# Kernel optimization log

Hardware: AMD Instinct MI355X
Metric: run time of the kernel (lower is better)

Reference implementation:

```python
import jax, jax.numpy as jnp
import numpy as np

B, T, D = 2, 2048, 1024
NH, NKV, HD, RD = 16, 4, 64, 32


def apply_rope(x, cos, sin):
    # x: [B, H, T, hd]; cos/sin: [T, 1, 1, RD//2]
    r = cos.shape[-1] * 2
    x1 = x[..., : r // 2]
    x2 = x[..., r // 2 : r]
    x_pass = x[..., r:]
    c = cos.reshape(1, 1, cos.shape[0], -1)  # [1,1,T,RD//2]
    s = sin.reshape(1, 1, sin.shape[0], -1)
    return jnp.concatenate([x1 * c - x2 * s, x1 * s + x2 * c, x_pass], axis=-1)


def setup_inputs() -> dict:
    key = jax.random.key(0)
    ks = jax.random.split(key, 8)
    # realistic partial-RoPE angle tables
    inv_freq = 1.0 / (10000.0 ** (np.arange(0, RD, 2, dtype=np.float32) / RD))
    ang = np.arange(T, dtype=np.float32)[:, None] * inv_freq[None, :]  # [T, RD//2]
    cos = jnp.asarray(np.cos(ang)).reshape(T, 1, 1, RD // 2)
    sin = jnp.asarray(np.sin(ang)).reshape(T, 1, 1, RD // 2)
    return {
        "x": jax.random.normal(ks[0], (B, T, D), dtype=jnp.float32),
        "cos": cos,
        "sin": sin,
        "v0": jax.random.normal(ks[1], (B, NH, T, HD), dtype=jnp.float32),
        "Wqkv": jax.random.normal(ks[2], ((NH + 2 * NKV) * HD, D), dtype=jnp.float32) * (D ** -0.5),
        "Wproj": jax.random.normal(ks[3], (D, D), dtype=jnp.float32) * (D ** -0.5),
        "vrl_alpha": jnp.full((NH,), 0.1, dtype=jnp.float32),
        "qk_scale": 0.5 + jax.random.uniform(ks[4], (NH,), dtype=jnp.float32),
    }


def reference(x, cos, sin, v0, Wqkv, Wproj, vrl_alpha, qk_scale):
    nH, nKV, hd = NH, NKV, HD
    qkv = jnp.einsum("btd,ed->bte", x, Wqkv)  # [B,T,(nH+2nKV)*hd]
    q = qkv[..., : nH * hd].reshape(B, T, nH, hd).transpose(0, 2, 1, 3)
    k = qkv[..., nH * hd : (nH + nKV) * hd].reshape(B, T, nKV, hd).transpose(0, 2, 1, 3)
    v = qkv[..., (nH + nKV) * hd :].reshape(B, T, nKV, hd).transpose(0, 2, 1, 3)
    q = apply_rope(q, cos, sin)
    k = apply_rope(k, cos, sin)
    reps = nH // nKV
    k_exp = jnp.repeat(k, reps, axis=1)  # [B,nH,T,hd]
    v_exp = jnp.repeat(v, reps, axis=1)
    # VRL blend (layer_idx > 0)
    alpha = jax.nn.sigmoid(vrl_alpha)[None, :, None, None]
    v_exp = (1.0 - alpha) * v_exp + alpha * v0
    # per-head learned qk scale, split as sqrt on q and k
    sfac = jnp.sqrt(qk_scale[None, :, None, None] * (hd ** -0.5))
    q_s = q * sfac
    k_s = k_exp * sfac
    # causal SDPA (default scale 1/sqrt(hd))
    scores = jnp.einsum("bhqd,bhkd->bhqk", q_s, k_s) * (hd ** -0.5)
    causal = jnp.tril(jnp.ones((T, T), dtype=bool))
    scores = jnp.where(causal[None, None], scores, jnp.float32(-1e30))
    attn = jax.nn.softmax(scores, axis=-1)
    y = jnp.einsum("bhqk,bhkd->bhqd", attn, v_exp)
    y = y.transpose(0, 2, 1, 3).reshape(B, T, D)
    out = jnp.einsum("btd,ed->bte", y, Wproj)
    return out, v0
```

## Files before the change

kernel.cpp:

```cpp
#include <hip/hip_runtime.h>
#include <hip/hip_bf16.h>

#define B_   2
#define T_   2048
#define D_   1024
#define NH_  16
#define NKV_ 4
#define HD_  64
#define E_   1536
#define LOG2E 1.4426950408889634f

typedef __attribute__((ext_vector_type(8))) __bf16 bf16x8;
typedef __attribute__((ext_vector_type(4))) __bf16 bf16x4;
typedef __attribute__((ext_vector_type(4))) float f32x4;

static __device__ __forceinline__ void gld_lds16(const unsigned short* g, unsigned short* l) {
  __builtin_amdgcn_global_load_lds(
      (const __attribute__((address_space(1))) unsigned int*)(unsigned long long)(const void*)g,
      (__attribute__((address_space(3))) unsigned int*)(unsigned int)(unsigned long long)(void*)l,
      16, 0, 0);
}

static __device__ __forceinline__ float fexp2(float x) {
  float r; asm("v_exp_f32 %0, %1" : "=v"(r) : "v"(x)); return r;
}
static __device__ __forceinline__ float fmax3(float a, float b, float c) {
  float r; asm("v_max3_f32 %0, %1, %2, %3" : "=v"(r) : "v"(a), "v"(b), "v"(c)); return r;
}
static __device__ __forceinline__ float frcp(float x) {
  float r; asm("v_rcp_f32 %0, %1" : "=v"(r) : "v"(x)); return r;
}

#define CVT8(dst, f0, f1) {                                                    \
  dst[0] = (__bf16)f0.x; dst[1] = (__bf16)f0.y;                               \
  dst[2] = (__bf16)f0.z; dst[3] = (__bf16)f0.w;                               \
  dst[4] = (__bf16)f1.x; dst[5] = (__bf16)f1.y;                               \
  dst[6] = (__bf16)f1.z; dst[7] = (__bf16)f1.w; }

__global__ void k_convert_all(const float* __restrict__ x, const float* __restrict__ wq,
                              const float* __restrict__ wp,
                              unsigned short* __restrict__ xb, unsigned short* __restrict__ wqb,
                              unsigned short* __restrict__ wpb) {
  int i = blockIdx.x * blockDim.x + threadIdx.x;
  const float* src; unsigned short* dst; int j;
  if (i < 524288)      { src = x;  dst = xb;  j = i; }
  else if (i < 720896) { src = wq; dst = wqb; j = i - 524288; }
  else                 { src = wp; dst = wpb; j = i - 720896; }
  int n = j >> 7, c8 = (j & 127) * 8;
  const float4* p = (const float4*)(src + (size_t)n * 1024 + c8);
  float4 a = p[0], b = p[1];
  bf16x8 o; CVT8(o, a, b);
  *(bf16x8*)(dst + (size_t)n * 1024 + (c8 ^ ((n & 7) * 8))) = o;
}

__global__ __launch_bounds__(256) void k_gemm_qkv(
    const unsigned short* __restrict__ A,
    const unsigned short* __restrict__ W,
    const float* __restrict__ cosT, const float* __restrict__ sinT,
    const float* __restrict__ v0,
    const float* __restrict__ vrl, const float* __restrict__ qks,
    unsigned short* __restrict__ qb, unsigned short* __restrict__ kb,
    unsigned short* __restrict__ vb) {
  __shared__ __align__(16) unsigned short As[2][128 * 64];
  __shared__ __align__(16) unsigned short Ws[2][64 * 64];
  int tid = threadIdx.x;
  int w = tid >> 6, l = tid & 63, lo = l & 15, hi = l >> 4;
  int f = blockIdx.y * 24 + blockIdx.x;
  int f2 = (f & 7) * 96 + (f >> 3);
  int bn = f2 % 24, bm = f2 / 24;
  int rsw = (lo & 7) * 8;

  const unsigned short* Ab = A + (size_t)bm * 128 * 1024;
  const unsigned short* Wb = W + (size_t)bn * 64 * 1024;

  f32x4 acc[2][4];
#pragma unroll
  for (int mi = 0; mi < 2; ++mi)
#pragma unroll
    for (int ni = 0; ni < 4; ++ni) acc[mi][ni] = (f32x4){0.f, 0.f, 0.f, 0.f};

#define STAGE(kt, buf) {                                                       \
  int k0 = (kt) * 64;                                                         \
  _Pragma("unroll") for (int ii = 0; ii < 4; ++ii) {                          \
    int sb = ii * 256 + w * 64;                                               \
    gld_lds16(Ab + (size_t)((sb + l) >> 3) * 1024 + k0 + ((sb + l) & 7) * 8,  \
              &As[buf][sb * 8]); }                                            \
  _Pragma("unroll") for (int ii = 0; ii < 2; ++ii) {                          \
    int sb = ii * 256 + w * 64;                                               \
    gld_lds16(Wb + (size_t)((sb + l) >> 3) * 1024 + k0 + ((sb + l) & 7) * 8,  \
              &Ws[buf][sb * 8]); } }

  STAGE(0, 0);
  __syncthreads();

  for (int kt = 0; kt < 16; ++kt) {
    int cur = kt & 1;
    bool pf = (kt + 1) < 16;
    if (pf) STAGE(kt + 1, cur ^ 1);
    __builtin_amdgcn_s_setprio(1);
#pragma unroll
    for (int kk = 0; kk < 2; ++kk) {
      int c0 = (kk * 32 + hi * 8) ^ rsw;
      bf16x8 af0 = *(const bf16x8*)&As[cur][(w * 32 + lo) * 64 + c0];
      bf16x8 af1 = *(const bf16x8*)&As[cur][(w * 32 + 16 + lo) * 64 + c0];
#pragma unroll
      for (int ni = 0; ni < 4; ++ni) {
        bf16x8 wf = *(const bf16x8*)&Ws[cur][(ni * 16 + lo) * 64 + c0];
        acc[0][ni] = __builtin_amdgcn_mfma_f32_16x16x32_bf16(af0, wf, acc[0][ni], 0, 0, 0);
        acc[1][ni] = __builtin_amdgcn_mfma_f32_16x16x32_bf16(af1, wf, acc[1][ni], 0, 0, 0);
      }
    }
    __builtin_amdgcn_s_setprio(0);
    __syncthreads();
  }
#undef STAGE

  if (bn < 20) {
    int isq = (bn < 16);
    int h = isq ? bn : bn - 16;
    float sc = isq ? (qks[h] * (LOG2E / 64.0f)) : 1.0f;
    unsigned short* base = isq ? qb : kb;
    int nheads = isq ? NH_ : NKV_;
#pragma unroll
    for (int mi = 0; mi < 2; ++mi) {
#pragma unroll
      for (int r = 0; r < 4; ++r) {
        int row = bm * 128 + w * 32 + mi * 16 + hi * 4 + r;
        int b = row >> 11, t = row & 2047;
        float c = cosT[t * 16 + lo], s = sinT[t * 16 + lo];
        float a0 = acc[mi][0][r], a1 = acc[mi][1][r];
        __bf16* dp = (__bf16*)(base + ((size_t)(b * nheads + h) * T_ + t) * 64);
        int ts = isq ? 0 : (8 * (t & 7));
        dp[lo ^ ts]        = (__bf16)((a0 * c - a1 * s) * sc);
        dp[(16 + lo) ^ ts] = (__bf16)((a0 * s + a1 * c) * sc);
        dp[(32 + lo) ^ ts] = (__bf16)(acc[mi][2][r] * sc);
        dp[(48 + lo) ^ ts] = (__bf16)(acc[mi][3][r] * sc);
      }
    }
  } else {
    int hv = bn - 20;
    float av[4];
#pragma unroll
    for (int j = 0; j < 4; ++j) av[j] = 1.0f / (1.0f + __expf(-vrl[hv * 4 + j]));
#pragma unroll
    for (int mi = 0; mi < 2; ++mi) {
      int t0g = bm * 128 + w * 32 + mi * 16 + hi * 4;
      int b = t0g >> 11, t0 = t0g & 2047;
#pragma unroll
      for (int ni = 0; ni < 4; ++ni) {
        int d = ni * 16 + lo;
#pragma unroll
        for (int j = 0; j < 4; ++j) {
          float a = av[j], na = 1.0f - a;
          const float* v0p = v0 + ((size_t)(b * NH_ + hv * 4 + j) * T_ + t0) * 64 + d;
          bf16x4 vv;
#pragma unroll
          for (int r = 0; r < 4; ++r)
            vv[r] = (__bf16)(na * acc[mi][ni][r] + a * v0p[(size_t)r * 64]);
          *(bf16x4*)((unsigned short*)vb + ((size_t)(b * NH_ + hv * 4 + j) * 64 + d) * T_ +
                     (t0 ^ (8 * (lo & 7)))) = vv;
        }
      }
    }
  }
}

__global__ __launch_bounds__(256) void k_gemm_proj(
    const unsigned short* __restrict__ A,
    const unsigned short* __restrict__ W,
    const float* __restrict__ v0,
    float* __restrict__ C, float* __restrict__ out2) {
  __shared__ __align__(16) unsigned short As[2][128 * 64];
  __shared__ __align__(16) unsigned short Ws[2][64 * 64];
  int tid = threadIdx.x;

  if (blockIdx.y >= 32) {
    int idx = ((blockIdx.y - 32) * 16 + blockIdx.x) * 256 + tid;
    const float4* src = (const float4*)v0;
    float4* dst = (float4*)out2;
#pragma unroll
    for (int i = 0; i < 32; ++i) dst[idx + i * 32768] = src[idx + i * 32768];
    return;
  }

  int w = tid >> 6, l = tid & 63, lo = l & 15, hi = l >> 4;
  int f = blockIdx.y * 16 + blockIdx.x;
  int f2 = (f & 7) * 64 + (f >> 3);
  int bn = f2 & 15, bm = f2 >> 4;
  int rsw = (lo & 7) * 8;

  const unsigned short* Ab = A + (size_t)bm * 128 * 1024;
  const unsigned short* Wb = W + (size_t)bn * 64 * 1024;

  f32x4 acc[2][4];
#pragma unroll
  for (int mi = 0; mi < 2; ++mi)
#pragma unroll
    for (int ni = 0; ni < 4; ++ni) acc[mi][ni] = (f32x4){0.f, 0.f, 0.f, 0.f};

#define STAGE(kt, buf) {                                                       \
  int k0 = (kt) * 64;                                                         \
  _Pragma("unroll") for (int ii = 0; ii < 4; ++ii) {                          \
    int sb = ii * 256 + w * 64;                                               \
    gld_lds16(Ab + (size_t)((sb + l) >> 3) * 1024 + k0 + ((sb + l) & 7) * 8,  \
              &As[buf][sb * 8]); }                                            \
  _Pragma("unroll") for (int ii = 0; ii < 2; ++ii) {                          \
    int sb = ii * 256 + w * 64;                                               \
    gld_lds16(Wb + (size_t)((sb + l) >> 3) * 1024 + k0 + ((sb + l) & 7) * 8,  \
              &Ws[buf][sb * 8]); } }

  STAGE(0, 0);
  __syncthreads();
  for (int kt = 0; kt < 16; ++kt) {
    int cur = kt & 1;
    bool pf = (kt + 1) < 16;
    if (pf) STAGE(kt + 1, cur ^ 1);
    __builtin_amdgcn_s_setprio(1);
#pragma unroll
    for (int kk = 0; kk < 2; ++kk) {
      int c0 = (kk * 32 + hi * 8) ^ rsw;
      bf16x8 af0 = *(const bf16x8*)&As[cur][(w * 32 + lo) * 64 + c0];
      bf16x8 af1 = *(const bf16x8*)&As[cur][(w * 32 + 16 + lo) * 64 + c0];
#pragma unroll
      for (int ni = 0; ni < 4; ++ni) {
        bf16x8 wf = *(const bf16x8*)&Ws[cur][(ni * 16 + lo) * 64 + c0];
        acc[0][ni] = __builtin_amdgcn_mfma_f32_16x16x32_bf16(af0, wf, acc[0][ni], 0, 0, 0);
        acc[1][ni] = __builtin_amdgcn_mfma_f32_16x16x32_bf16(af1, wf, acc[1][ni], 0, 0, 0);
      }
    }
    __builtin_amdgcn_s_setprio(0);
    __syncthreads();
  }
#undef STAGE

#pragma unroll
  for (int mi = 0; mi < 2; ++mi) {
#pragma unroll
    for (int r = 0; r < 4; ++r) {
      int row = bm * 128 + w * 32 + mi * 16 + hi * 4 + r;
      float* cp = C + (size_t)row * D_ + bn * 64 + lo;
#pragma unroll
      for (int ni = 0; ni < 4; ++ni) cp[ni * 16] = acc[mi][ni][r];
    }
  }
}

static __device__ __forceinline__ void stage_kv8(const unsigned short* Kb, const unsigned short* Vb,
                                                 int kv0, int w, int l,
                                                 unsigned short* KsB, unsigned short* VsB) {
  gld_lds16(Kb + (size_t)kv0 * 64 + w * 512 + l * 8, KsB + w * 512);
  gld_lds16(Vb + (size_t)(w * 8 + (l >> 3)) * T_ + kv0 + (l & 7) * 8, VsB + w * 512);
}

__device__ __forceinline__ void softmax_state(f32x4 (&s)[4], float& m, float& lsum,
                                              f32x4 (&y)[4], unsigned short* PsW,
                                              int lo, int hi, int swz) {
  float a0 = fmax3(s[0][0], s[0][1], s[0][2]);
  float a1 = fmax3(s[0][3], s[1][0], s[1][1]);
  float a2 = fmax3(s[1][2], s[1][3], s[2][0]);
  float a3 = fmax3(s[2][1], s[2][2], s[2][3]);
  float a4 = fmax3(s[3][0], s[3][1], s[3][2]);
  float pm = fmaxf(fmax3(a0, a1, a2), fmax3(a3, a4, s[3][3]));
  if (!__all(pm <= m + 8.0f)) {
    pm = fmaxf(pm, __shfl_xor(pm, 16));
    pm = fmaxf(pm, __shfl_xor(pm, 32));
    float mnew = fmaxf(m, pm);
    float sc = fexp2(m - mnew);
    lsum *= sc;
#pragma unroll
    for (int r = 0; r < 4; ++r) {
      float scr = __shfl(sc, hi * 4 + r);
#pragma unroll
      for (int nf = 0; nf < 4; ++nf) y[nf][r] *= scr;
    }
    m = mnew;
  }
  float rs = 0.f;
#pragma unroll
  for (int nt = 0; nt < 4; ++nt) {
    float p0 = fexp2(s[nt][0] - m);
    float p1 = fexp2(s[nt][1] - m);
    float p2 = fexp2(s[nt][2] - m);
    float p3 = fexp2(s[nt][3] - m);
    rs += (p0 + p1) + (p2 + p3);
    bf16x4 pk;
    pk[0] = (__bf16)p0; pk[1] = (__bf16)p1; pk[2] = (__bf16)p2; pk[3] = (__bf16)p3;
    *(bf16x4*)(PsW + lo * 64 + ((nt * 16 + hi * 4) ^ swz)) = pk;
  }
  lsum += rs;
}

__global__ __launch_bounds__(512, 4) void k_attn(const unsigned short* __restrict__ Q,
                                                 const unsigned short* __restrict__ Kp,
                                                 const unsigned short* __restrict__ Vtp,
                                                 unsigned short* __restrict__ Y) {
  int p = blockIdx.x, h = blockIdx.y, b = blockIdx.z;
  if (b == 1) p = 15 - p;
  int tid = threadIdx.x;
  int w = tid >> 6, l = tid & 63, lo = l & 15, hi = l >> 4;
  int kh = h >> 2;
  int qtA = p, qtB = 31 - p;
  int ntB = qtB + 1;
  int st = w >> 2, wq = w & 3;
  int qt = st ? qtA : qtB;
  int q0 = qt * 64 + wq * 16;
  int swz = 8 * (lo & 7);

  __shared__ __align__(16) unsigned short Ks[2][4096];
  __shared__ __align__(16) unsigned short Vs[2][4096];
  __shared__ __align__(16) unsigned short Ps[8192];
  unsigned short* PsW = &Ps[w * 1024];

  const unsigned short* Qb = Q + ((size_t)(b * NH_ + h) * T_) * 64;
  const unsigned short* Kb = Kp + ((size_t)(b * NKV_ + kh) * T_) * 64;
  const unsigned short* Vb = Vtp + ((size_t)(b * NH_ + h) * 64) * T_;

  bf16x8 q_0 = *(const bf16x8*)(Qb + (size_t)(q0 + lo) * 64 + hi * 8);
  bf16x8 q_1 = *(const bf16x8*)(Qb + (size_t)(q0 + lo) * 64 + 32 + hi * 8);

  f32x4 y[4];
#pragma unroll
  for (int nf = 0; nf < 4; ++nf) y[nf] = (f32x4){0.f, 0.f, 0.f, 0.f};
  float m = -INFINITY, lsum = 0.f;

  stage_kv8(Kb, Vb, 0, w, l, Ks[0], Vs[0]);
  __syncthreads();
  int cur = 0;

  for (int kt = 0; kt < ntB; ++kt) {
    bool pf = (kt + 1) < ntB;
    if (pf) stage_kv8(Kb, Vb, (kt + 1) * 64, w, l, Ks[cur ^ 1], Vs[cur ^ 1]);

    if (kt <= qt) {
      int kv0 = kt * 64;
      const unsigned short* KsC = Ks[cur];
      const unsigned short* VsC = Vs[cur];

      f32x4 s[4];
      __builtin_amdgcn_s_setprio(1);
#pragma unroll
      for (int nt = 0; nt < 4; ++nt) {
        int rrow = (nt * 16 + lo) * 64;
        int c0 = (hi * 8) ^ swz;
        bf16x8 kf0 = *(const bf16x8*)&KsC[rrow + c0];
        bf16x8 kf1 = *(const bf16x8*)&KsC[rrow + (c0 ^ 32)];
        f32x4 a = (f32x4){0.f, 0.f, 0.f, 0.f};
        a = __builtin_amdgcn_mfma_f32_16x16x32_bf16(kf0, q_0, a, 0, 0, 0);
        a = __builtin_amdgcn_mfma_f32_16x16x32_bf16(kf1, q_1, a, 0, 0, 0);
        s[nt] = a;
      }
      __builtin_amdgcn_s_setprio(0);

      if (kt == qt) {
#pragma unroll
        for (int nt = 0; nt < 4; ++nt)
#pragma unroll
          for (int r = 0; r < 4; ++r)
            if (kv0 + nt * 16 + hi * 4 + r > q0 + lo) s[nt][r] = -1e30f;
      }

      softmax_state(s, m, lsum, y, PsW, lo, hi, swz);

      __builtin_amdgcn_s_setprio(1);
#pragma unroll
      for (int kc = 0; kc < 2; ++kc) {
        int pcol = (kc * 32 + hi * 8) ^ swz;
        bf16x8 pa = *(const bf16x8*)&PsW[lo * 64 + pcol];
#pragma unroll
        for (int nf = 0; nf < 4; ++nf) {
          bf16x8 vf = *(const bf16x8*)&VsC[(nf * 16 + lo) * 64 + pcol];
          y[nf] = __builtin_amdgcn_mfma_f32_16x16x32_bf16(pa, vf, y[nf], 0, 0, 0);
        }
      }
      __builtin_amdgcn_s_setprio(0);
    }

    __syncthreads();
    cur ^= 1;
  }

  lsum += __shfl_xor(lsum, 16);
  lsum += __shfl_xor(lsum, 32);
  float inv = frcp(lsum);
#pragma unroll
  for (int r = 0; r < 4; ++r) {
    float iv = __shfl(inv, hi * 4 + r);
    int t = q0 + hi * 4 + r;
    int sw = 8 * (t & 7);
    __bf16* yp = (__bf16*)(Y + ((size_t)(b * T_ + t)) * D_ + h * 64);
#pragma unroll
    for (int nf = 0; nf < 4; ++nf)
      yp[(nf * 16 + lo) ^ sw] = (__bf16)(y[nf][r] * iv);
  }
}

extern "C" void kernel_launch(void* const* d_in, const int* in_sizes, int n_in,
                              void* d_out, int out_size, void* d_ws, size_t ws_size,
                              hipStream_t stream) {
  const float* x     = (const float*)d_in[0];
  const float* cosT  = (const float*)d_in[1];
  const float* sinT  = (const float*)d_in[2];
  const float* v0    = (const float*)d_in[3];
  const float* Wqkv  = (const float*)d_in[4];
  const float* Wproj = (const float*)d_in[5];
  const float* vrl   = (const float*)d_in[6];
  const float* qks   = (const float*)d_in[7];
  float* out = (float*)d_out;

  char* ws = (char*)d_ws;
  unsigned short* xb     = (unsigned short*)ws;
  unsigned short* wqkvb  = (unsigned short*)(ws + 8388608);
  unsigned short* wprojb = (unsigned short*)(ws + 11534336);
  unsigned short* qb     = (unsigned short*)(ws + 13631488);
  unsigned short* kb     = (unsigned short*)(ws + 22020096);
  unsigned short* vb     = (unsigned short*)(ws + 24117248);
  unsigned short* yb     = (unsigned short*)(ws + 32505856);

  k_convert_all<<<3328, 256, 0, stream>>>(x, Wqkv, Wproj, xb, wqkvb, wprojb);

  k_gemm_qkv<<<dim3(24, 32), 256, 0, stream>>>(xb, wqkvb, cosT, sinT, v0, vrl, qks, qb, kb, vb);

  k_attn<<<dim3(16, NH_, B_), 512, 0, stream>>>(qb, kb, vb, yb);

  k_gemm_proj<<<dim3(16, 40), 256, 0, stream>>>(yb, wprojb, v0, out, out + 4194304);
}
```

Measured before the change: 96.20 us.

## Enlarge GEMM tiles to 128x128 and triple-buffer attention K/V with waitcnt barriers

Both GEMM kernels move from 128x64 to 128x128 output tiles with a 2x2 wave layout, so each wave computes a 64x64 sub-tile with 16 accumulators. This raises MFMA work per LDS fragment load and halves the block count. The attention kernel switches from double to triple buffering of K/V, issuing loads two tiles ahead and syncing with explicit vmcnt waits plus s_barrier instead of __syncthreads. Its launch bound drops to 2 blocks per SM to allow for the larger LDS and register use. Risks are lower occupancy and fewer blocks (384 for QKV, 256 for proj) to fill the CUs.

```diff
diff --git a/kernel.cpp b/kernel.cpp
--- a/kernel.cpp
+++ b/kernel.cpp
@@ -30,6 +30,11 @@
 static __device__ __forceinline__ float frcp(float x) {
   float r; asm("v_rcp_f32 %0, %1" : "=v"(r) : "v"(x)); return r;
 }
+
+#define PIPE_BARRIER(N) {                                   \
+  asm volatile("s_waitcnt vmcnt(" #N ")" ::: "memory");     \
+  __builtin_amdgcn_s_barrier();                             \
+  __builtin_amdgcn_sched_barrier(0); }
 
 #define CVT8(dst, f0, f1) {                                                    \
   dst[0] = (__bf16)f0.x; dst[1] = (__bf16)f0.y;                               \
@@ -62,33 +67,36 @@
     unsigned short* __restrict__ qb, unsigned short* __restrict__ kb,
     unsigned short* __restrict__ vb) {
   __shared__ __align__(16) unsigned short As[2][128 * 64];
-  __shared__ __align__(16) unsigned short Ws[2][64 * 64];
+  __shared__ __align__(16) unsigned short Ws[2][128 * 64];
   int tid = threadIdx.x;
   int w = tid >> 6, l = tid & 63, lo = l & 15, hi = l >> 4;
-  int f = blockIdx.y * 24 + blockIdx.x;
-  int f2 = (f & 7) * 96 + (f >> 3);
-  int bn = f2 % 24, bm = f2 / 24;
+  int wm = w >> 1, wn = w & 1;
+  int f = blockIdx.y * 12 + blockIdx.x;
+  int f2 = (f & 7) * 48 + (f >> 3);
+  int bn = f2 % 12, bm = f2 / 12;
   int rsw = (lo & 7) * 8;
 
   const unsigned short* Ab = A + (size_t)bm * 128 * 1024;
-  const unsigned short* Wb = W + (size_t)bn * 64 * 1024;
-
-  f32x4 acc[2][4];
-#pragma unroll
-  for (int mi = 0; mi < 2; ++mi)
+  const unsigned short* Wb = W + (size_t)bn * 128 * 1024;
+
+  f32x4 acc[4][4];
+#pragma unroll
+  for (int mi = 0; mi < 4; ++mi)
 #pragma unroll
     for (int ni = 0; ni < 4; ++ni) acc[mi][ni] = (f32x4){0.f, 0.f, 0.f, 0.f};
 
 #define STAGE(kt, buf) {                                                       \
   int k0 = (kt) * 64;                                                         \
   _Pragma("unroll") for (int ii = 0; ii < 4; ++ii) {                          \
-    int sb = ii * 256 + w * 64;                                               \
-    gld_lds16(Ab + (size_t)((sb + l) >> 3) * 1024 + k0 + ((sb + l) & 7) * 8,  \
-              &As[buf][sb * 8]); }                                            \
-  _Pragma("unroll") for (int ii = 0; ii < 2; ++ii) {                          \
-    int sb = ii * 256 + w * 64;                                               \
-    gld_lds16(Wb + (size_t)((sb + l) >> 3) * 1024 + k0 + ((sb + l) & 7) * 8,  \
-              &Ws[buf][sb * 8]); } }
+    int sb = ii * 256 + tid;                                                  \
+    gld_lds16(Ab + (size_t)(sb >> 3) * 1024 + k0 + (sb & 7) * 8,              \
+              &As[buf][(sb & ~63) * 8]);                                      \
+  }                                                                           \
+  _Pragma("unroll") for (int ii = 0; ii < 4; ++ii) {                          \
+    int sb = ii * 256 + tid;                                                  \
+    gld_lds16(Wb + (size_t)(sb >> 3) * 1024 + k0 + (sb & 7) * 8,              \
+              &Ws[buf][(sb & ~63) * 8]);                                      \
+  } }
 
   STAGE(0, 0);
   __syncthreads();
@@ -101,31 +109,36 @@
 #pragma unroll
     for (int kk = 0; kk < 2; ++kk) {
       int c0 = (kk * 32 + hi * 8) ^ rsw;
-      bf16x8 af0 = *(const bf16x8*)&As[cur][(w * 32 + lo) * 64 + c0];
-      bf16x8 af1 = *(const bf16x8*)&As[cur][(w * 32 + 16 + lo) * 64 + c0];
-#pragma unroll
-      for (int ni = 0; ni < 4; ++ni) {
-        bf16x8 wf = *(const bf16x8*)&Ws[cur][(ni * 16 + lo) * 64 + c0];
-        acc[0][ni] = __builtin_amdgcn_mfma_f32_16x16x32_bf16(af0, wf, acc[0][ni], 0, 0, 0);
-        acc[1][ni] = __builtin_amdgcn_mfma_f32_16x16x32_bf16(af1, wf, acc[1][ni], 0, 0, 0);
-      }
+      bf16x8 af[4], wf[4];
+#pragma unroll
+      for (int mi = 0; mi < 4; ++mi)
+        af[mi] = *(const bf16x8*)&As[cur][(wm * 64 + mi * 16 + lo) * 64 + c0];
+#pragma unroll
+      for (int ni = 0; ni < 4; ++ni)
+        wf[ni] = *(const bf16x8*)&Ws[cur][(wn * 64 + ni * 16 + lo) * 64 + c0];
+#pragma unroll
+      for (int mi = 0; mi < 4; ++mi)
+#pragma unroll
+        for (int ni = 0; ni < 4; ++ni)
+          acc[mi][ni] = __builtin_amdgcn_mfma_f32_16x16x32_bf16(af[mi], wf[ni], acc[mi][ni], 0, 0, 0);
     }
     __builtin_amdgcn_s_setprio(0);
     __syncthreads();
   }
 #undef STAGE
 
-  if (bn < 20) {
-    int isq = (bn < 16);
-    int h = isq ? bn : bn - 16;
+  int hg = bn * 2 + wn;
+  if (hg < 20) {
+    int isq = (hg < 16);
+    int h = isq ? hg : hg - 16;
     float sc = isq ? (qks[h] * (LOG2E / 64.0f)) : 1.0f;
     unsigned short* base = isq ? qb : kb;
     int nheads = isq ? NH_ : NKV_;
 #pragma unroll
-    for (int mi = 0; mi < 2; ++mi) {
+    for (int mi = 0; mi < 4; ++mi) {
 #pragma unroll
       for (int r = 0; r < 4; ++r) {
-        int row = bm * 128 + w * 32 + mi * 16 + hi * 4 + r;
+        int row = bm * 128 + wm * 64 + mi * 16 + hi * 4 + r;
         int b = row >> 11, t = row & 2047;
         float c = cosT[t * 16 + lo], s = sinT[t * 16 + lo];
         float a0 = acc[mi][0][r], a1 = acc[mi][1][r];
@@ -138,13 +151,13 @@
       }
     }
   } else {
-    int hv = bn - 20;
+    int hv = hg - 20;
     float av[4];
 #pragma unroll
     for (int j = 0; j < 4; ++j) av[j] = 1.0f / (1.0f + __expf(-vrl[hv * 4 + j]));
 #pragma unroll
-    for (int mi = 0; mi < 2; ++mi) {
-      int t0g = bm * 128 + w * 32 + mi * 16 + hi * 4;
+    for (int mi = 0; mi < 4; ++mi) {
+      int t0g = bm * 128 + wm * 64 + mi * 16 + hi * 4;
       int b = t0g >> 11, t0 = t0g & 2047;
 #pragma unroll
       for (int ni = 0; ni < 4; ++ni) {
@@ -171,11 +184,11 @@
     const float* __restrict__ v0,
     float* __restrict__ C, float* __restrict__ out2) {
   __shared__ __align__(16) unsigned short As[2][128 * 64];
-  __shared__ __align__(16) unsigned short Ws[2][64 * 64];
+  __shared__ __align__(16) unsigned short Ws[2][128 * 64];
   int tid = threadIdx.x;
 
   if (blockIdx.y >= 32) {
-    int idx = ((blockIdx.y - 32) * 16 + blockIdx.x) * 256 + tid;
+    int idx = ((blockIdx.y - 32) * 8 + blockIdx.x) * 256 + tid;
     const float4* src = (const float4*)v0;
     float4* dst = (float4*)out2;
 #pragma unroll
@@ -184,30 +197,33 @@
   }
 
   int w = tid >> 6, l = tid & 63, lo = l & 15, hi = l >> 4;
-  int f = blockIdx.y * 16 + blockIdx.x;
-  int f2 = (f & 7) * 64 + (f >> 3);
-  int bn = f2 & 15, bm = f2 >> 4;
+  int wm = w >> 1, wn = w & 1;
+  int f = blockIdx.y * 8 + blockIdx.x;
+  int f2 = (f & 7) * 32 + (f >> 3);
+  int bn = f2 & 7, bm = f2 >> 3;
   int rsw = (lo & 7) * 8;
 
   const unsigned short* Ab = A + (size_t)bm * 128 * 1024;
-  const unsigned short* Wb = W + (size_t)bn * 64 * 1024;
-
-  f32x4 acc[2][4];
-#pragma unroll
-  for (int mi = 0; mi < 2; ++mi)
+  const unsigned short* Wb = W + (size_t)bn * 128 * 1024;
+
+  f32x4 acc[4][4];
+#pragma unroll
+  for (int mi = 0; mi < 4; ++mi)
 #pragma unroll
     for (int ni = 0; ni < 4; ++ni) acc[mi][ni] = (f32x4){0.f, 0.f, 0.f, 0.f};
 
 #define STAGE(kt, buf) {                                                       \
   int k0 = (kt) * 64;                                                         \
   _Pragma("unroll") for (int ii = 0; ii < 4; ++ii) {                          \
-    int sb = ii * 256 + w * 64;                                               \
-    gld_lds16(Ab + (size_t)((sb + l) >> 3) * 1024 + k0 + ((sb + l) & 7) * 8,  \
-              &As[buf][sb * 8]); }                                            \
-  _Pragma("unroll") for (int ii = 0; ii < 2; ++ii) {                          \
-    int sb = ii * 256 + w * 64;                                               \
-    gld_lds16(Wb + (size_t)((sb + l) >> 3) * 1024 + k0 + ((sb + l) & 7) * 8,  \
-              &Ws[buf][sb * 8]); } }
+    int sb = ii * 256 + tid;                                                  \
+    gld_lds16(Ab + (size_t)(sb >> 3) * 1024 + k0 + (sb & 7) * 8,              \
+              &As[buf][(sb & ~63) * 8]);                                      \
+  }                                                                           \
+  _Pragma("unroll") for (int ii = 0; ii < 4; ++ii) {                          \
+    int sb = ii * 256 + tid;                                                  \
+    gld_lds16(Wb + (size_t)(sb >> 3) * 1024 + k0 + (sb & 7) * 8,              \
+              &Ws[buf][(sb & ~63) * 8]);                                      \
+  } }
 
   STAGE(0, 0);
   __syncthreads();
@@ -219,14 +235,18 @@
 #pragma unroll
     for (int kk = 0; kk < 2; ++kk) {
       int c0 = (kk * 32 + hi * 8) ^ rsw;
-      bf16x8 af0 = *(const bf16x8*)&As[cur][(w * 32 + lo) * 64 + c0];
-      bf16x8 af1 = *(const bf16x8*)&As[cur][(w * 32 + 16 + lo) * 64 + c0];
-#pragma unroll
-      for (int ni = 0; ni < 4; ++ni) {
-        bf16x8 wf = *(const bf16x8*)&Ws[cur][(ni * 16 + lo) * 64 + c0];
-        acc[0][ni] = __builtin_amdgcn_mfma_f32_16x16x32_bf16(af0, wf, acc[0][ni], 0, 0, 0);
-        acc[1][ni] = __builtin_amdgcn_mfma_f32_16x16x32_bf16(af1, wf, acc[1][ni], 0, 0, 0);
-      }
+      bf16x8 af[4], wf[4];
+#pragma unroll
+      for (int mi = 0; mi < 4; ++mi)
+        af[mi] = *(const bf16x8*)&As[cur][(wm * 64 + mi * 16 + lo) * 64 + c0];
+#pragma unroll
+      for (int ni = 0; ni < 4; ++ni)
+        wf[ni] = *(const bf16x8*)&Ws[cur][(wn * 64 + ni * 16 + lo) * 64 + c0];
+#pragma unroll
+      for (int mi = 0; mi < 4; ++mi)
+#pragma unroll
+        for (int ni = 0; ni < 4; ++ni)
+          acc[mi][ni] = __builtin_amdgcn_mfma_f32_16x16x32_bf16(af[mi], wf[ni], acc[mi][ni], 0, 0, 0);
     }
     __builtin_amdgcn_s_setprio(0);
     __syncthreads();
@@ -234,11 +254,11 @@
 #undef STAGE
 
 #pragma unroll
-  for (int mi = 0; mi < 2; ++mi) {
+  for (int mi = 0; mi < 4; ++mi) {
 #pragma unroll
     for (int r = 0; r < 4; ++r) {
-      int row = bm * 128 + w * 32 + mi * 16 + hi * 4 + r;
-      float* cp = C + (size_t)row * D_ + bn * 64 + lo;
+      int row = bm * 128 + wm * 64 + mi * 16 + hi * 4 + r;
+      float* cp = C + (size_t)row * D_ + bn * 128 + wn * 64 + lo;
 #pragma unroll
       for (int ni = 0; ni < 4; ++ni) cp[ni * 16] = acc[mi][ni][r];
     }
@@ -290,7 +310,7 @@
   lsum += rs;
 }
 
-__global__ __launch_bounds__(512, 4) void k_attn(const unsigned short* __restrict__ Q,
+__global__ __launch_bounds__(512, 2) void k_attn(const unsigned short* __restrict__ Q,
                                                  const unsigned short* __restrict__ Kp,
                                                  const unsigned short* __restrict__ Vtp,
                                                  unsigned short* __restrict__ Y) {
@@ -306,8 +326,8 @@
   int q0 = qt * 64 + wq * 16;
   int swz = 8 * (lo & 7);
 
-  __shared__ __align__(16) unsigned short Ks[2][4096];
-  __shared__ __align__(16) unsigned short Vs[2][4096];
+  __shared__ __align__(16) unsigned short Ks[3][4096];
+  __shared__ __align__(16) unsigned short Vs[3][4096];
   __shared__ __align__(16) unsigned short Ps[8192];
   unsigned short* PsW = &Ps[w * 1024];
 
@@ -324,12 +344,12 @@
   float m = -INFINITY, lsum = 0.f;
 
   stage_kv8(Kb, Vb, 0, w, l, Ks[0], Vs[0]);
-  __syncthreads();
-  int cur = 0;
+  stage_kv8(Kb, Vb, 64, w, l, Ks[1], Vs[1]);
+  int cur = 0, wbuf = 2;
 
   for (int kt = 0; kt < ntB; ++kt) {
-    bool pf = (kt + 1) < ntB;
-    if (pf) stage_kv8(Kb, Vb, (kt + 1) * 64, w, l, Ks[cur ^ 1], Vs[cur ^ 1]);
+    if (kt + 1 < ntB) PIPE_BARRIER(2) else PIPE_BARRIER(0);
+    if (kt + 2 < ntB) stage_kv8(Kb, Vb, (kt + 2) * 64, w, l, Ks[wbuf], Vs[wbuf]);
 
     if (kt <= qt) {
       int kv0 = kt * 64;
@@ -375,8 +395,8 @@
       __builtin_amdgcn_s_setprio(0);
     }
 
-    __syncthreads();
-    cur ^= 1;
+    cur = (cur == 2) ? 0 : cur + 1;
+    wbuf = (wbuf == 2) ? 0 : wbuf + 1;
   }
 
   lsum += __shfl_xor(lsum, 16);
@@ -418,9 +438,9 @@
 
   k_convert_all<<<3328, 256, 0, stream>>>(x, Wqkv, Wproj, xb, wqkvb, wprojb);
 
-  k_gemm_qkv<<<dim3(24, 32), 256, 0, stream>>>(xb, wqkvb, cosT, sinT, v0, vrl, qks, qb, kb, vb);
+  k_gemm_qkv<<<dim3(12, 32), 256, 0, stream>>>(xb, wqkvb, cosT, sinT, v0, vrl, qks, qb, kb, vb);
 
   k_attn<<<dim3(16, NH_, B_), 512, 0, stream>>>(qb, kb, vb, yb);
 
-  k_gemm_proj<<<dim3(16, 40), 256, 0, stream>>>(yb, wprojb, v0, out, out + 4194304);
-}
+  k_gemm_proj<<<dim3(8, 48), 256, 0, stream>>>(yb, wprojb, v0, out, out + 4194304);
+}
```

Result: faster. 91.90 us (-4.5%).
